# Kernel tuning notes

Measured on AMD Instinct MI355X. Metric: run time of the kernel, lower is better.

## Reference

```python
import jax, jax.numpy as jnp
import numpy as np

B, C, H, W = 16, 512, 32, 32
NUM_GROUPS = 32
EPS = 1e-5


def setup_inputs() -> dict:
    key = jax.random.key(0)
    ks = jax.random.split(key, 7)
    x = jax.random.normal(ks[0], (B, C, H, W), dtype=jnp.float32)
    gamma = jnp.ones((C,), dtype=jnp.float32)
    beta = jnp.zeros((C,), dtype=jnp.float32)
    # project_in: Conv2d(C, 3C, 1) -> weight [3C, C], bias [3C]
    w_in = jax.random.normal(ks[1], (3 * C, C), dtype=jnp.float32) / np.sqrt(C)
    b_in = jnp.zeros((3 * C,), dtype=jnp.float32)
    # project_out: Conv2d(C, C, 1) with init_scale=0.0 -> zero-init in original;
    # use small random weights so gradients/outputs are non-trivial for testing.
    w_out = jax.random.normal(ks[2], (C, C), dtype=jnp.float32) / np.sqrt(C)
    b_out = jnp.zeros((C,), dtype=jnp.float32)
    return {"x": x, "gamma": gamma, "beta": beta, "w_in": w_in, "b_in": b_in,
            "w_out": w_out, "b_out": b_out}


def group_norm(x, gamma, beta):
    b, c, h, w = x.shape
    xg = x.reshape(b, NUM_GROUPS, c // NUM_GROUPS, h, w)
    mean = xg.mean(axis=(2, 3, 4), keepdims=True)
    var = xg.var(axis=(2, 3, 4), keepdims=True)
    xn = ((xg - mean) * jax.lax.rsqrt(var + EPS)).reshape(b, c, h, w)
    return xn * gamma[None, :, None, None] + beta[None, :, None, None]


def reference(x, gamma, beta, w_in, b_in, w_out, b_out):
    skip = x  # in_channels == out_channels -> Identity skip
    xn = group_norm(x, gamma, beta)
    # 1x1 conv == channel matmul
    qkv = jnp.einsum('oc,bchw->bohw', w_in, xn) + b_in[None, :, None, None]
    q, k, v = jnp.split(qkv, 3, axis=1)  # each [B, C, H, W]
    cm = q.shape[1]
    # [B, H, W, H*W] scores
    scores = jnp.einsum('bchw,bcHW->bhwHW', q, k).reshape(B, H, W, H * W)
    attn = jax.nn.softmax(scores / jnp.sqrt(jnp.float32(cm)), axis=-1)
    attn = attn.reshape(B, H, W, H, W)
    out = jnp.einsum('bhwHW,bcHW->bchw', attn, v)
    out = jnp.einsum('oc,bchw->bohw', w_out, out) + b_out[None, :, None, None]
    return out + skip
```

## Files before the change

### kernel.cpp

```cpp
#include <hip/hip_runtime.h>
#include <hip/hip_bf16.h>
#include <cstdint>
#include <cstddef>

#define HW   1024
#define NC   512
#define NB   16
#define EPSV 1e-5f

typedef __hip_bfloat16 bf16;
typedef __attribute__((ext_vector_type(8))) __bf16 bf16x8;
typedef __attribute__((ext_vector_type(4))) float f32x4;

__device__ __forceinline__ float b2f(bf16 h) { return __bfloat162float(h); }

__device__ __forceinline__ void gload16(const void* g, void* l) {
  __builtin_amdgcn_global_load_lds(
      (const __attribute__((address_space(1))) uint32_t*)g,
      (__attribute__((address_space(3))) uint32_t*)l, 16, 0, 0);
}

__global__ __launch_bounds__(256) void cvt_w_kernel(
    const float* __restrict__ wi, const float* __restrict__ wo,
    bf16* __restrict__ wib, bf16* __restrict__ wob) {
  int i = blockIdx.x * 256 + threadIdx.x;
  const float4* src;
  bf16* dst;
  int j;
  if (i < 196608) { src = (const float4*)wi; j = i; dst = wib; }
  else            { src = (const float4*)wo; j = i - 196608; dst = wob; }
  float4 v = src[j];
  union { bf16 h[4]; uint2 u; } p;
  p.h[0] = __float2bfloat16(v.x); p.h[1] = __float2bfloat16(v.y);
  p.h[2] = __float2bfloat16(v.z); p.h[3] = __float2bfloat16(v.w);
  *(uint2*)&dst[(size_t)j * 4] = p.u;
}

__global__ __launch_bounds__(256) void gn_kernel(
    const float* __restrict__ x, const float* __restrict__ gamma,
    const float* __restrict__ beta, bf16* __restrict__ xn) {
  int blk = blockIdx.x;
  int b = blk >> 5, g = blk & 31;
  size_t base = ((size_t)(b * NC + g * 16)) * HW;
  const float4* src4 = (const float4*)(x + base);
  int t = threadIdx.x;
  float s = 0.f, ss = 0.f;
  float4 v[16];
#pragma unroll
  for (int i = 0; i < 16; ++i) {
    v[i] = src4[t + i * 256];
    s  += v[i].x + v[i].y + v[i].z + v[i].w;
    ss += v[i].x * v[i].x + v[i].y * v[i].y + v[i].z * v[i].z + v[i].w * v[i].w;
  }
  __shared__ float red[256];
  red[t] = s; __syncthreads();
  for (int o = 128; o > 0; o >>= 1) { if (t < o) red[t] += red[t + o]; __syncthreads(); }
  float mean = red[0] * (1.f / 16384.f);
  __syncthreads();
  red[t] = ss; __syncthreads();
  for (int o = 128; o > 0; o >>= 1) { if (t < o) red[t] += red[t + o]; __syncthreads(); }
  float var = red[0] * (1.f / 16384.f) - mean * mean;
  float rstd = rsqrtf(var + EPSV);

  __shared__ bf16 sm[16][1032];
#pragma unroll
  for (int i = 0; i < 16; ++i) {
    int idx = t + i * 256;
    int c = idx >> 8;
    int hw4 = (idx & 255) * 4;
    float gm = gamma[g * 16 + c], bt = beta[g * 16 + c];
    union { bf16 h[4]; uint2 u; } p;
    p.h[0] = __float2bfloat16((v[i].x - mean) * rstd * gm + bt);
    p.h[1] = __float2bfloat16((v[i].y - mean) * rstd * gm + bt);
    p.h[2] = __float2bfloat16((v[i].z - mean) * rstd * gm + bt);
    p.h[3] = __float2bfloat16((v[i].w - mean) * rstd * gm + bt);
    *(uint2*)&sm[c][hw4] = p.u;
  }
  __syncthreads();
  bf16* dst = xn + (size_t)b * HW * NC + g * 16;
#pragma unroll
  for (int it = 0; it < 8; ++it) {
    int u = it * 256 + t;
    int hw = u >> 1;
    int c8 = (u & 1) * 8;
    union { bf16 h[8]; uint4 q; } p;
#pragma unroll
    for (int j = 0; j < 8; ++j) p.h[j] = sm[c8 + j][hw];
    *(uint4*)&dst[(size_t)hw * NC + c8] = p.q;
  }
}

template <int MODE>
__global__ __launch_bounds__(256) void gemm_bt(
    const bf16* __restrict__ A, int lda, long long sA,
    const bf16* __restrict__ B, int ldb, long long sB,
    void* __restrict__ Cv, int ldc, long long sC,
    int K,
    const float* __restrict__ bias,
    const float* __restrict__ resid, long long sR,
    float scale) {
  __shared__ bf16 sT[2][128][32];
  int z = blockIdx.z;
  const bf16* Ab = A + (size_t)z * sA;
  const bf16* Bb = B + (size_t)z * sB;
  int n0 = blockIdx.x * 128, m0 = blockIdx.y * 128;
  int t = threadIdx.x;
  int l = t & 63, w = t >> 6;
  int wm = w >> 1, wn = w & 1;

  int srow = t >> 2;
  int scol = (t & 3) * 8;

  f32x4 acc[4][4] = {};

  const bf16* ga0 = Ab + (size_t)(m0 + srow) * lda + scol;
  const bf16* gb0 = Bb + (size_t)(n0 + srow) * ldb + scol;

  for (int k0 = 0; k0 < K; k0 += 32) {
    gload16(ga0 + k0, &sT[0][srow][scol]);
    gload16(ga0 + (size_t)64 * lda + k0, &sT[0][64 + srow][scol]);
    gload16(gb0 + k0, &sT[1][srow][scol]);
    gload16(gb0 + (size_t)64 * ldb + k0, &sT[1][64 + srow][scol]);
    __syncthreads();
    bf16x8 af[4], bfr[4];
    int kc = (l >> 4) * 8;
    int ra = wm * 64 + (l & 15);
    int rb = wn * 64 + (l & 15);
#pragma unroll
    for (int i = 0; i < 4; ++i) {
      af[i]  = *(const bf16x8*)&sT[0][ra + i * 16][kc];
      bfr[i] = *(const bf16x8*)&sT[1][rb + i * 16][kc];
    }
#pragma unroll
    for (int i = 0; i < 4; ++i)
#pragma unroll
      for (int j = 0; j < 4; ++j)
        acc[i][j] = __builtin_amdgcn_mfma_f32_16x16x32_bf16(af[i], bfr[j], acc[i][j], 0, 0, 0);
    __syncthreads();
  }

  int rbase = (l >> 4) * 4;
#pragma unroll
  for (int i = 0; i < 4; ++i) {
    int row = m0 + wm * 64 + i * 16 + rbase;
    float4 bv = make_float4(0.f, 0.f, 0.f, 0.f);
    if (MODE == 0 || MODE == 3) bv = *(const float4*)&bias[row];
    else if (MODE == 1) { if (bias) bv = *(const float4*)&bias[row]; }
#pragma unroll
    for (int j = 0; j < 4; ++j) {
      int col = n0 + wn * 64 + j * 16 + (l & 15);
      if (MODE == 0) {
        bf16* C = (bf16*)Cv + (size_t)z * sC;
        union { bf16 h[4]; uint2 u; } p;
        p.h[0] = __float2bfloat16(acc[i][j][0] + bv.x);
        p.h[1] = __float2bfloat16(acc[i][j][1] + bv.y);
        p.h[2] = __float2bfloat16(acc[i][j][2] + bv.z);
        p.h[3] = __float2bfloat16(acc[i][j][3] + bv.w);
        *(uint2*)&C[(size_t)col * ldc + row] = p.u;
      } else if (MODE == 1) {
        bf16* C = (bf16*)Cv + (size_t)z * sC;
        float bb[4] = {bv.x, bv.y, bv.z, bv.w};
#pragma unroll
        for (int r = 0; r < 4; ++r)
          C[(size_t)(row + r) * ldc + col] = __float2bfloat16(acc[i][j][r] + bb[r]);
      } else {
        float* C = (float*)Cv + (size_t)z * sC;
        float bb[4] = {bv.x, bv.y, bv.z, bv.w};
#pragma unroll
        for (int r = 0; r < 4; ++r) {
          size_t off = (size_t)(row + r) * ldc + col;
          C[off] = acc[i][j][r] + bb[r] + resid[(size_t)z * sR + off];
        }
      }
    }
  }
}

__global__ __launch_bounds__(512, 1) void flash_kernel(
    const bf16* __restrict__ qk, const bf16* __restrict__ vcm,
    bf16* __restrict__ ao) {
  __shared__ char lds[163840];
  char* Qs  = lds;
  char* Kb0 = lds + 65536;
  char* Kb1 = lds + 81920;
  char* Vs  = lds + 98304;

  int id = blockIdx.x;
  int xcd = id & 7, rest = id >> 3;
  int q = rest & 15, bh = rest >> 4;
  int b = xcd + bh * 8;
  int i0 = q * 64;

  const char* qkC = (const char*)qk + (size_t)b * 2097152;
  const char* vC  = (const char*)vcm + (size_t)b * 1048576;
  bf16* aob = ao + (size_t)b * (HW * NC) + (size_t)i0 * NC;

  int t = threadIdx.x, l = t & 63, w = t >> 6;
  int l15 = l & 15, lq = l >> 4;
  int jg = w >> 1, ih = w & 1;
  int chb = w * 64;

  auto stage_k = [&](int tile_, int c_, char* dst_) {
#pragma unroll
    for (int qq = 0; qq < 2; ++qq) {
      int drow = w * 8 + qq * 4 + lq;
      int cb = l15 * 16;
      gload16(qkC + (size_t)(tile_ * 64 + drow) * 2048 + 1024 + c_ * 256
                  + (cb ^ ((drow & 7) << 4)),
              dst_ + w * 2048 + qq * 1024 + l * 16);
    }
  };
  auto stage_v = [&](int tile_, int v_) {
    int ch = v_ * 64 + w * 8 + (l >> 3);
    int cb = (l & 7) * 16;
    gload16(vC + (size_t)ch * 2048 + tile_ * 128 + (cb ^ ((ch & 7) << 4)),
            Vs + v_ * 8192 + w * 1024 + l * 16);
  };

  {
    const char* qbase = qkC + (size_t)i0 * 2048;
#pragma unroll
    for (int it = 0; it < 8; ++it) {
      int s = it * 8192 + t * 16;
      int i = s >> 10, wb = s & 1023;
      gload16(qbase + (size_t)i * 2048 + (wb ^ ((i & 7) << 4)), Qs + s);
    }
  }
  stage_k(0, 0, Kb0);

  float lacc[2] = {0.f, 0.f};
  f32x4 o[4][4] = {};
  const float scl = 0.044194173824159216f;

  __syncthreads();

  for (int tile = 0; tile < 16; ++tile) {
    char* PsBuf = (tile & 1) ? Kb1 : Kb0;
    f32x4 s[2] = {};
#pragma unroll
    for (int p = 0; p < 4; ++p) {
      if (p < 3) {
        char* kd = ((p + 1 + tile) & 1) ? Kb1 : Kb0;
        stage_k(tile, p + 1, kd);
      }
      stage_v(tile, p * 2);
      stage_v(tile, p * 2 + 1);
      const char* kcur = ((p + tile) & 1) ? Kb1 : Kb0;
      int krow = jg * 16 + l15;
#pragma unroll
      for (int k2 = 0; k2 < 4; ++k2) {
        bf16x8 kf = *(const bf16x8*)(kcur + krow * 256
                      + ((k2 * 64 + lq * 16) ^ ((krow & 7) << 4)));
#pragma unroll
        for (int ni = 0; ni < 2; ++ni) {
          int i = ih * 32 + ni * 16 + l15;
          bf16x8 qf = *(const bf16x8*)(Qs + i * 1024
                        + ((p * 256 + k2 * 64 + lq * 16) ^ ((i & 7) << 4)));
          s[ni] = __builtin_amdgcn_mfma_f32_16x16x32_bf16(kf, qf, s[ni], 0, 0, 0);
        }
      }
      __syncthreads();
    }
#pragma unroll
    for (int ni = 0; ni < 2; ++ni) {
      int i = ih * 32 + ni * 16 + l15;
      float p0 = __expf(s[ni][0] * scl);
      float p1 = __expf(s[ni][1] * scl);
      float p2 = __expf(s[ni][2] * scl);
      float p3 = __expf(s[ni][3] * scl);
      lacc[ni] += p0 + p1 + p2 + p3;
      union { bf16 h[4]; uint64_t u; } pk;
      pk.h[0] = __float2bfloat16(p0); pk.h[1] = __float2bfloat16(p1);
      pk.h[2] = __float2bfloat16(p2); pk.h[3] = __float2bfloat16(p3);
      *(uint64_t*)(PsBuf + i * 128 + ((jg * 32 + lq * 8) ^ ((i & 7) << 4))) = pk.u;
    }
    __syncthreads();
    if (tile < 15) {
      char* kd = ((tile + 1) & 1) ? Kb1 : Kb0;
      stage_k(tile + 1, 0, kd);
    }
#pragma unroll
    for (int ks = 0; ks < 2; ++ks) {
      bf16x8 vf[4];
#pragma unroll
      for (int mi = 0; mi < 4; ++mi) {
        int ch = chb + mi * 16 + l15;
        vf[mi] = *(const bf16x8*)(Vs + ch * 128
                   + ((ks * 64 + lq * 16) ^ ((ch & 7) << 4)));
      }
#pragma unroll
      for (int ni = 0; ni < 4; ++ni) {
        int i = ni * 16 + l15;
        bf16x8 pf = *(const bf16x8*)(PsBuf + i * 128
                      + ((ks * 64 + lq * 16) ^ ((i & 7) << 4)));
#pragma unroll
        for (int mi = 0; mi < 4; ++mi)
          o[mi][ni] = __builtin_amdgcn_mfma_f32_16x16x32_bf16(vf[mi], pf, o[mi][ni], 0, 0, 0);
      }
    }
    __syncthreads();
  }

  float* redl = (float*)Qs;
#pragma unroll
  for (int ni = 0; ni < 2; ++ni) {
    float v = lacc[ni];
    v += __shfl_xor(v, 16);
    v += __shfl_xor(v, 32);
    if (l < 16) redl[jg * 64 + ih * 32 + ni * 16 + l] = v;
  }
  __syncthreads();
  float linv[4];
#pragma unroll
  for (int ni = 0; ni < 4; ++ni) {
    int i = ni * 16 + l15;
    linv[ni] = 1.f / (redl[i] + redl[64 + i] + redl[128 + i] + redl[192 + i]);
  }
#pragma unroll
  for (int mi = 0; mi < 4; ++mi)
#pragma unroll
    for (int ni = 0; ni < 4; ++ni) {
      union { bf16 h[4]; uint64_t u; } pk;
#pragma unroll
      for (int r = 0; r < 4; ++r)
        pk.h[r] = __float2bfloat16(o[mi][ni][r] * linv[ni]);
      int i = ni * 16 + l15;
      int ch = chb + mi * 16 + lq * 4;
      *(uint64_t*)(aob + (size_t)i * NC + ch) = pk.u;
    }
}

extern "C" void kernel_launch(void* const* d_in, const int* in_sizes, int n_in,
                              void* d_out, int out_size, void* d_ws, size_t ws_size,
                              hipStream_t stream) {
  const float* x     = (const float*)d_in[0];
  const float* gamma = (const float*)d_in[1];
  const float* beta  = (const float*)d_in[2];
  const float* w_in  = (const float*)d_in[3];
  const float* b_in  = (const float*)d_in[4];
  const float* w_out = (const float*)d_in[5];
  const float* b_out = (const float*)d_in[6];
  float* out = (float*)d_out;

  char* w = (char*)d_ws;
  bf16* xn  = (bf16*)w;
  bf16* ao  = xn;
  bf16* qk  = (bf16*)(w + ((size_t)16 << 20));
  bf16* vcm = (bf16*)(w + ((size_t)48 << 20));
  bf16* wib = (bf16*)(w + ((size_t)64 << 20));
  bf16* wob = (bf16*)(w + ((size_t)64 << 20) + ((size_t)3 << 19));

  cvt_w_kernel<<<1024, 256, 0, stream>>>(w_in, w_out, wib, wob);
  gn_kernel<<<NB * 32, 256, 0, stream>>>(x, gamma, beta, xn);

  gemm_bt<0><<<dim3(8, 8, NB), 256, 0, stream>>>(
      wib, 512, 0, xn, 512, 512 * 1024, qk, 1024, 1024 * 1024, 512,
      b_in, nullptr, 0, 0.f);
  gemm_bt<1><<<dim3(8, 4, NB), 256, 0, stream>>>(
      wib + 1024 * 512, 512, 0, xn, 512, 512 * 1024, vcm, 1024, 512 * 1024, 512,
      b_in + 1024, nullptr, 0, 0.f);

  flash_kernel<<<256, 512, 0, stream>>>(qk, vcm, ao);

  gemm_bt<3><<<dim3(8, 4, NB), 256, 0, stream>>>(
      wob, 512, 0, ao, 512, 524288, out, 1024, 524288, 512,
      b_out, x, 524288, 0.f);
}
```

Baseline: 154.4 us.

## Fuse output projection, bias and residual into the flash attention kernel

```diff
diff --git a/kernel.cpp b/kernel.cpp
--- a/kernel.cpp
+++ b/kernel.cpp
@@ -96,9 +96,7 @@
     const bf16* __restrict__ B, int ldb, long long sB,
     void* __restrict__ Cv, int ldc, long long sC,
     int K,
-    const float* __restrict__ bias,
-    const float* __restrict__ resid, long long sR,
-    float scale) {
+    const float* __restrict__ bias) {
   __shared__ bf16 sT[2][128][32];
   int z = blockIdx.z;
   const bf16* Ab = A + (size_t)z * sA;
@@ -144,7 +142,7 @@
   for (int i = 0; i < 4; ++i) {
     int row = m0 + wm * 64 + i * 16 + rbase;
     float4 bv = make_float4(0.f, 0.f, 0.f, 0.f);
-    if (MODE == 0 || MODE == 3) bv = *(const float4*)&bias[row];
+    if (MODE == 0) bv = *(const float4*)&bias[row];
     else if (MODE == 1) { if (bias) bv = *(const float4*)&bias[row]; }
 #pragma unroll
     for (int j = 0; j < 4; ++j) {
@@ -157,20 +155,12 @@
         p.h[2] = __float2bfloat16(acc[i][j][2] + bv.z);
         p.h[3] = __float2bfloat16(acc[i][j][3] + bv.w);
         *(uint2*)&C[(size_t)col * ldc + row] = p.u;
-      } else if (MODE == 1) {
+      } else {
         bf16* C = (bf16*)Cv + (size_t)z * sC;
         float bb[4] = {bv.x, bv.y, bv.z, bv.w};
 #pragma unroll
         for (int r = 0; r < 4; ++r)
           C[(size_t)(row + r) * ldc + col] = __float2bfloat16(acc[i][j][r] + bb[r]);
-      } else {
-        float* C = (float*)Cv + (size_t)z * sC;
-        float bb[4] = {bv.x, bv.y, bv.z, bv.w};
-#pragma unroll
-        for (int r = 0; r < 4; ++r) {
-          size_t off = (size_t)(row + r) * ldc + col;
-          C[off] = acc[i][j][r] + bb[r] + resid[(size_t)z * sR + off];
-        }
       }
     }
   }
@@ -178,12 +168,16 @@
 
 __global__ __launch_bounds__(512, 1) void flash_kernel(
     const bf16* __restrict__ qk, const bf16* __restrict__ vcm,
-    bf16* __restrict__ ao) {
+    const bf16* __restrict__ wout, const float* __restrict__ b_out,
+    const float* __restrict__ x, float* __restrict__ out) {
   __shared__ char lds[163840];
   char* Qs  = lds;
   char* Kb0 = lds + 65536;
   char* Kb1 = lds + 81920;
   char* Vs  = lds + 98304;
+  char* Wb0 = lds + 65536;
+  char* Wb1 = lds + 98304;
+  float* redl = (float*)(lds + 131072);
 
   int id = blockIdx.x;
   int xcd = id & 7, rest = id >> 3;
@@ -193,7 +187,7 @@
 
   const char* qkC = (const char*)qk + (size_t)b * 2097152;
   const char* vC  = (const char*)vcm + (size_t)b * 1048576;
-  bf16* aob = ao + (size_t)b * (HW * NC) + (size_t)i0 * NC;
+  const char* wC  = (const char*)wout;
 
   int t = threadIdx.x, l = t & 63, w = t >> 6;
   int l15 = l & 15, lq = l >> 4;
@@ -215,6 +209,15 @@
     int cb = (l & 7) * 16;
     gload16(vC + (size_t)ch * 2048 + tile_ * 128 + (cb ^ ((ch & 7) << 4)),
             Vs + v_ * 8192 + w * 1024 + l * 16);
+  };
+  auto stage_w = [&](int kc_, char* dst_) {
+#pragma unroll
+    for (int it = 0; it < 4; ++it) {
+      int idx = it * 512 + t;
+      int row = idx >> 2, cb = (idx & 3) * 16;
+      gload16(wC + (size_t)row * 1024 + kc_ * 64 + (cb ^ ((row & 3) << 4)),
+              dst_ + idx * 16);
+    }
   };
 
   {
@@ -301,7 +304,7 @@
     __syncthreads();
   }
 
-  float* redl = (float*)Qs;
+  stage_w(0, Wb0);
 #pragma unroll
   for (int ni = 0; ni < 2; ++ni) {
     float v = lacc[ni];
@@ -325,9 +328,51 @@
       for (int r = 0; r < 4; ++r)
         pk.h[r] = __float2bfloat16(o[mi][ni][r] * linv[ni]);
       int i = ni * 16 + l15;
-      int ch = chb + mi * 16 + lq * 4;
-      *(uint64_t*)(aob + (size_t)i * NC + ch) = pk.u;
-    }
+      int c2 = (chb + mi * 16 + lq * 4) * 2;
+      *(uint64_t*)(Qs + i * 1024 + (c2 ^ ((i & 7) << 4))) = pk.u;
+    }
+  __syncthreads();
+
+  f32x4 acc2[4][4] = {};
+#pragma unroll
+  for (int kc = 0; kc < 16; ++kc) {
+    if (kc < 15) stage_w(kc + 1, ((kc + 1) & 1) ? Wb1 : Wb0);
+    const char* Wc = (kc & 1) ? Wb1 : Wb0;
+    bf16x8 wf[4];
+#pragma unroll
+    for (int mi = 0; mi < 4; ++mi) {
+      int row = chb + mi * 16 + l15;
+      wf[mi] = *(const bf16x8*)(Wc + row * 64 + ((lq * 16) ^ ((row & 3) << 4)));
+    }
+#pragma unroll
+    for (int ni = 0; ni < 4; ++ni) {
+      int i = ni * 16 + l15;
+      bf16x8 pf = *(const bf16x8*)(Qs + i * 1024
+                    + ((kc * 64 + lq * 16) ^ ((i & 7) << 4)));
+#pragma unroll
+      for (int mi = 0; mi < 4; ++mi)
+        acc2[mi][ni] = __builtin_amdgcn_mfma_f32_16x16x32_bf16(wf[mi], pf, acc2[mi][ni], 0, 0, 0);
+    }
+    __syncthreads();
+  }
+
+  const float* xb = x + (size_t)b * 524288;
+  float* ob = out + (size_t)b * 524288;
+#pragma unroll
+  for (int mi = 0; mi < 4; ++mi) {
+    int cbase = chb + mi * 16 + lq * 4;
+    float4 bv = *(const float4*)&b_out[cbase];
+    float bb[4] = {bv.x, bv.y, bv.z, bv.w};
+#pragma unroll
+    for (int ni = 0; ni < 4; ++ni) {
+      int i = i0 + ni * 16 + l15;
+#pragma unroll
+      for (int r = 0; r < 4; ++r) {
+        size_t off = (size_t)(cbase + r) * 1024 + i;
+        ob[off] = acc2[mi][ni][r] + bb[r] + xb[off];
+      }
+    }
+  }
 }
 
 extern "C" void kernel_launch(void* const* d_in, const int* in_sizes, int n_in,
@@ -344,7 +389,6 @@
 
   char* w = (char*)d_ws;
   bf16* xn  = (bf16*)w;
-  bf16* ao  = xn;
   bf16* qk  = (bf16*)(w + ((size_t)16 << 20));
   bf16* vcm = (bf16*)(w + ((size_t)48 << 20));
   bf16* wib = (bf16*)(w + ((size_t)64 << 20));
@@ -354,15 +398,10 @@
   gn_kernel<<<NB * 32, 256, 0, stream>>>(x, gamma, beta, xn);
 
   gemm_bt<0><<<dim3(8, 8, NB), 256, 0, stream>>>(
-      wib, 512, 0, xn, 512, 512 * 1024, qk, 1024, 1024 * 1024, 512,
-      b_in, nullptr, 0, 0.f);
+      wib, 512, 0, xn, 512, 512 * 1024, qk, 1024, 1024 * 1024, 512, b_in);
   gemm_bt<1><<<dim3(8, 4, NB), 256, 0, stream>>>(
       wib + 1024 * 512, 512, 0, xn, 512, 512 * 1024, vcm, 1024, 512 * 1024, 512,
-      b_in + 1024, nullptr, 0, 0.f);
-
-  flash_kernel<<<256, 512, 0, stream>>>(qk, vcm, ao);
-
-  gemm_bt<3><<<dim3(8, 4, NB), 256, 0, stream>>>(
-      wob, 512, 0, ao, 512, 524288, out, 1024, 524288, 512,
-      b_out, x, 524288, 0.f);
-}
+      b_in + 1024);
+
+  flash_kernel<<<256, 512, 0, stream>>>(qk, vcm, wob, b_out, x, out);
+}
```

After: 146.7 us. 1.05x faster.
